# Performance work log

Measured on AMD Instinct MI355X. Metric: run time of the kernel, lower is better.

Reference implementation:

```python
import jax, jax.numpy as jnp
import numpy as np

ALPHA = 100.0
EPS = 1e-12  # matches torch F.normalize eps


def l2norm(v, axis):
    n = jnp.linalg.norm(v, axis=axis, keepdims=True)
    return v / jnp.maximum(n, EPS)


def setup_inputs() -> dict:
    key = jax.random.key(0)
    k1, k2 = jax.random.split(key)
    x = jax.random.normal(k1, (32, 512, 32, 32), dtype=jnp.float32)
    vocabs = jax.random.uniform(k2, (64, 512), dtype=jnp.float32)  # torch.rand init
    return {"x": x, "vocabs": vocabs}


def reference(x, vocabs):
    # x: [N, C, H, W]; vocabs: [K, C]
    N, C, H, W = x.shape
    K = vocabs.shape[0]
    x = l2norm(x, axis=1)                       # normalize descriptors over C
    xf = x.reshape(N, C, H * W)                 # [N, C, P]

    # 1x1 conv with weight = 2*alpha*vocabs, bias = -alpha*||vocabs||
    w = 2.0 * ALPHA * vocabs                    # [K, C]
    b = -ALPHA * jnp.linalg.norm(vocabs, axis=1)  # [K]
    logits = jnp.einsum('ncp,kc->nkp', xf, w) + b[None, :, None]
    a = jax.nn.softmax(logits, axis=1)          # soft assignment over K

    # Distributive rewrite of sum_p a[n,k,p]*(x[n,c,p] - vocabs[k,c])
    vlad = jnp.einsum('nkp,ncp->nkc', a, xf) - a.sum(-1)[:, :, None] * vocabs[None]
    vlad = l2norm(vlad, axis=2)                 # intra-normalization
    vlad = vlad.reshape(N, K * C)
    return l2norm(vlad, axis=1)
```

## Files before the change

### kernel.cpp

```cpp
#include <hip/hip_runtime.h>
#include <math.h>
#include <stdint.h>

#define ALPHA 100.0f
#define EPSN 1e-12f

typedef __attribute__((ext_vector_type(8))) short bf16x8;
typedef __attribute__((ext_vector_type(16))) float f32x16;
typedef __attribute__((ext_vector_type(4))) float f32x4;
typedef __attribute__((ext_vector_type(4))) unsigned int u32x4;

static __device__ __forceinline__ uint32_t f2bf(float f) {
    uint32_t u = __builtin_bit_cast(uint32_t, f);
    return (u + 0x7FFFu + ((u >> 16) & 1u)) >> 16;
}
static __device__ __forceinline__ float bfhi(uint32_t u) {
    return __builtin_bit_cast(float, u & 0xFFFF0000u);
}
static __device__ __forceinline__ uint32_t packbf(float a, float b) {
    return f2bf(a) | (f2bf(b) << 16);
}
static __device__ __forceinline__ void lds_barrier() {
    asm volatile("s_waitcnt lgkmcnt(0)\n\ts_barrier" ::: "memory");
}

__global__ __launch_bounds__(64) void prep_kernel(const float* __restrict__ v,
                                                  unsigned short* __restrict__ vh,
                                                  unsigned short* __restrict__ vl,
                                                  float* __restrict__ bias,
                                                  float* __restrict__ az) {
    int k = blockIdx.x, lane = threadIdx.x;
    az[k * 64 + lane] = 0.f;
    const float* row = v + k * 512;
    float ssq = 0.f;
#pragma unroll
    for (int i = 0; i < 8; ++i) {
        int c = lane + 64 * i;
        float f = row[c];
        ssq = fmaf(f, f, ssq);
        uint32_t hi = f2bf(f);
        uint32_t lo = f2bf(f - __builtin_bit_cast(float, hi << 16));
        vh[k * 512 + c] = (unsigned short)hi;
        vl[k * 512 + c] = (unsigned short)lo;
    }
#pragma unroll
    for (int off = 32; off > 0; off >>= 1) ssq += __shfl_xor(ssq, off, 64);
    if (lane == 0) bias[k] = -ALPHA * sqrtf(ssq);
}

__global__ __launch_bounds__(256) void assign_kernel(
    const float* __restrict__ x, const unsigned short* __restrict__ vh,
    const unsigned short* __restrict__ vl, const float* __restrict__ bias,
    unsigned short* __restrict__ aT, float* __restrict__ asum) {
    __shared__ uint32_t xph[4][2][16 * 36];
    __shared__ uint32_t xpl[4][2][16 * 36];
    __shared__ float ssqw[4][32];
    __shared__ float bias_l[64];
    __shared__ float xch[2][2][32];

    int tid = threadIdx.x, bx = blockIdx.x;
    int n = bx >> 4, pblk = (bx & 15) << 6;
    int l = tid & 63, w = tid >> 6;
    int kh = w & 1, ph = w >> 1;
    int h = l >> 5, cl = l & 31;
    int c8 = l & 7, j = (l >> 3) & 7;

    if (tid < 64) bias_l[tid] = bias[tid];

    const float* xg = x + (size_t)n * 524288 + pblk + 32 * ph + 4 * c8;
    const unsigned short* vhg = vh + (size_t)(32 * kh + cl) * 512 + 8 * h;
    const unsigned short* vlg = vl + (size_t)(32 * kh + cl) * 512 + 8 * h;

    uint32_t* bh0 = xph[w][0];
    uint32_t* bh1 = xph[w][1];
    uint32_t* bl0 = xpl[w][0];
    uint32_t* bl1 = xpl[w][1];

    f32x16 acc;
#pragma unroll
    for (int r = 0; r < 16; ++r) acc[r] = 0.f;
    f32x4 ssqv;
#pragma unroll
    for (int i = 0; i < 4; ++i) ssqv[i] = 0.f;

    float4 xv[2][4];
    u32x4 vfh[2][2], vfl[2][2];

#define A_LOADX(slot, c0)                                                      \
    {                                                                          \
        xv[slot][0] = *(const float4*)(xg + (size_t)((c0) + 2 * j) * 1024);    \
        xv[slot][1] = *(const float4*)(xg + (size_t)((c0) + 2 * j + 1) * 1024);\
        xv[slot][2] = *(const float4*)(xg + (size_t)((c0) + 2 * j + 16) * 1024);\
        xv[slot][3] = *(const float4*)(xg + (size_t)((c0) + 2 * j + 17) * 1024);\
    }
#define A_LOADV(slot, c0)                                                      \
    {                                                                          \
        vfh[slot][0] = *(const u32x4*)(vhg + (c0));                            \
        vfh[slot][1] = *(const u32x4*)(vhg + (c0) + 16);                       \
        vfl[slot][0] = *(const u32x4*)(vlg + (c0));                            \
        vfl[slot][1] = *(const u32x4*)(vlg + (c0) + 16);                       \
    }
#define A_STAGE(bh_, bl_, slot)                                                \
    {                                                                          \
        _Pragma("unroll") for (int ps0 = 0; ps0 < 2; ++ps0) {                  \
            float fa[4] = {xv[slot][2 * ps0].x, xv[slot][2 * ps0].y,           \
                           xv[slot][2 * ps0].z, xv[slot][2 * ps0].w};          \
            float fb[4] = {xv[slot][2 * ps0 + 1].x, xv[slot][2 * ps0 + 1].y,   \
                           xv[slot][2 * ps0 + 1].z, xv[slot][2 * ps0 + 1].w};  \
            u32x4 hp, lp;                                                      \
            _Pragma("unroll") for (int i = 0; i < 4; ++i) {                    \
                uint32_t h0 = f2bf(fa[i]);                                     \
                uint32_t l0 = f2bf(fa[i] - bfhi(h0 << 16));                    \
                uint32_t h1 = f2bf(fb[i]);                                     \
                uint32_t l1 = f2bf(fb[i] - bfhi(h1 << 16));                    \
                hp[i] = h0 | (h1 << 16);                                       \
                lp[i] = l0 | (l1 << 16);                                       \
                ssqv[i] = fmaf(fa[i], fa[i], fmaf(fb[i], fb[i], ssqv[i]));     \
            }                                                                  \
            *(u32x4*)&(bh_)[(j + 8 * ps0) * 36 + 4 * c8] = hp;                 \
            *(u32x4*)&(bl_)[(j + 8 * ps0) * 36 + 4 * c8] = lp;                 \
        }                                                                      \
    }
#define A_COMPUTE(bh_, bl_, slot)                                              \
    {                                                                          \
        _Pragma("unroll") for (int s = 0; s < 2; ++s) {                        \
            int xb = (8 * s + 4 * h) * 36 + cl;                                \
            u32x4 bhp, blp;                                                    \
            _Pragma("unroll") for (int q = 0; q < 4; ++q) {                    \
                bhp[q] = (bh_)[xb + q * 36];                                   \
                blp[q] = (bl_)[xb + q * 36];                                   \
            }                                                                  \
            bf16x8 ah = __builtin_bit_cast(bf16x8, vfh[slot][s]);              \
            bf16x8 al = __builtin_bit_cast(bf16x8, vfl[slot][s]);              \
            bf16x8 xbh = __builtin_bit_cast(bf16x8, bhp);                      \
            bf16x8 xbl = __builtin_bit_cast(bf16x8, blp);                      \
            acc = __builtin_amdgcn_mfma_f32_32x32x16_bf16(ah, xbh, acc, 0, 0, 0);\
            acc = __builtin_amdgcn_mfma_f32_32x32x16_bf16(ah, xbl, acc, 0, 0, 0);\
            acc = __builtin_amdgcn_mfma_f32_32x32x16_bf16(al, xbh, acc, 0, 0, 0);\
        }                                                                      \
    }

    A_LOADX(0, 0);
    A_LOADV(0, 0);
    A_LOADX(1, 32);
    A_LOADV(1, 32);
    __syncthreads();
    A_STAGE(bh0, bl0, 0);
#pragma unroll
    for (int i = 0; i < 16; ++i) {
        if ((i & 1) == 0) {
            A_COMPUTE(bh0, bl0, 0);
            if (i < 15) A_STAGE(bh1, bl1, 1);
            if (i < 14) {
                A_LOADX(0, (i + 2) * 32);
                A_LOADV(0, (i + 2) * 32);
            }
        } else {
            A_COMPUTE(bh1, bl1, 1);
            if (i < 15) A_STAGE(bh0, bl0, 0);
            if (i < 14) {
                A_LOADX(1, (i + 2) * 32);
                A_LOADV(1, (i + 2) * 32);
            }
        }
    }
#undef A_LOADX
#undef A_LOADV
#undef A_STAGE
#undef A_COMPUTE

#pragma unroll
    for (int i = 0; i < 4; ++i) {
        float v = ssqv[i];
        v += __shfl_xor(v, 8, 64);
        v += __shfl_xor(v, 16, 64);
        v += __shfl_xor(v, 32, 64);
        ssqv[i] = v;
    }
    if (l < 8) *(f32x4*)&ssqw[w][4 * c8] = ssqv;
    float ssq = ssqw[w][cl];

    float sinv = 1.0f / fmaxf(sqrtf(ssq), EPSN);
    float twoAs = 2.0f * ALPHA * sinv;
    float e[16];
    float m = -INFINITY;
#pragma unroll
    for (int r = 0; r < 16; ++r) {
        int k = (r & 3) + 8 * (r >> 2) + 4 * h + 32 * kh;
        float lv = fmaf(twoAs, acc[r], bias_l[k]);
        e[r] = lv;
        m = fmaxf(m, lv);
    }
    m = fmaxf(m, __shfl_xor(m, 32, 64));
    __syncthreads();
    if (l < 32) xch[kh][ph][l] = m;
    __syncthreads();
    m = fmaxf(m, xch[1 - kh][ph][cl]);
    float ssum = 0.f;
#pragma unroll
    for (int r = 0; r < 16; ++r) {
        e[r] = expf(e[r] - m);
        ssum += e[r];
    }
    ssum += __shfl_xor(ssum, 32, 64);
    __syncthreads();
    if (l < 32) xch[kh][ph][l] = ssum;
    __syncthreads();
    ssum += xch[1 - kh][ph][cl];
    float rs = 1.0f / ssum;
    float a2s = rs * sinv;
    unsigned short* aTn = aT + (size_t)n * 65536 + pblk + 32 * ph + cl;
#pragma unroll
    for (int r = 0; r < 16; ++r) {
        int k = (r & 3) + 8 * (r >> 2) + 4 * h + 32 * kh;
        aTn[(size_t)k * 1024] = (unsigned short)f2bf(e[r] * a2s);
        float red = e[r] * rs;
#pragma unroll
        for (int off = 1; off <= 16; off <<= 1) red += __shfl_xor(red, off, 64);
        if (cl == 0) atomicAdd(&asum[n * 64 + k], red);
    }
}

static __device__ __forceinline__ void v_load(float4& qxa, float4& qxb,
                                              u32x4& qa0, u32x4& qa1,
                                              const float* xg,
                                              const unsigned short* ag, int p0) {
    qxa = *(const float4*)(xg + p0);
    qxb = *(const float4*)(xg + p0 + 32);
    qa0 = *(const u32x4*)(ag + p0);
    qa1 = *(const u32x4*)(ag + p0 + 8);
}
static __device__ __forceinline__ void v_stage(uint32_t* xtb, uint32_t* atb,
                                               const float4 qxa, const float4 qxb,
                                               const u32x4 qa0, const u32x4 qa1,
                                               int xr, int xq, int ak, int aj) {
    int xb = xr * 34 + (xq >> 1);
    *(uint2*)&xtb[xb] = make_uint2(packbf(qxa.x, qxa.y), packbf(qxa.z, qxa.w));
    *(uint2*)&xtb[xb + 16] = make_uint2(packbf(qxb.x, qxb.y), packbf(qxb.z, qxb.w));
    int ab = ak * 34 + (aj >> 1);
    *(uint2*)&atb[ab] = make_uint2(qa0[0], qa0[1]);
    *(uint2*)&atb[ab + 2] = make_uint2(qa0[2], qa0[3]);
    *(uint2*)&atb[ab + 4] = make_uint2(qa1[0], qa1[1]);
    *(uint2*)&atb[ab + 6] = make_uint2(qa1[2], qa1[3]);
}
static __device__ __forceinline__ void v_compute(const uint32_t* xtb,
                                                 const uint32_t* atb,
                                                 f32x16& acc, int kh, int h,
                                                 int cl) {
#pragma unroll
    for (int s = 0; s < 4; ++s) {
        int va = (32 * kh + cl) * 34 + 8 * s + 4 * h;
        uint2 f0 = *(const uint2*)&atb[va];
        uint2 f1 = *(const uint2*)&atb[va + 2];
        int vb = cl * 34 + 8 * s + 4 * h;
        uint2 g0 = *(const uint2*)&xtb[vb];
        uint2 g1 = *(const uint2*)&xtb[vb + 2];
        u32x4 afp, bfp;
        afp[0] = f0.x; afp[1] = f0.y; afp[2] = f1.x; afp[3] = f1.y;
        bfp[0] = g0.x; bfp[1] = g0.y; bfp[2] = g1.x; bfp[3] = g1.y;
        acc = __builtin_amdgcn_mfma_f32_32x32x16_bf16(
            __builtin_bit_cast(bf16x8, afp), __builtin_bit_cast(bf16x8, bfp),
            acc, 0, 0, 0);
    }
}

__global__ __launch_bounds__(256) void vlad_kernel(
    const float* __restrict__ x, const unsigned short* __restrict__ aT,
    const float* __restrict__ asum, const float* __restrict__ vocabs,
    float* __restrict__ out, float* __restrict__ knorm) {
    __shared__ uint32_t xt[2][32 * 34];
    __shared__ uint32_t at[2][64 * 34];
    __shared__ float cmb[2][64][16];
    __shared__ float asum_l[64];

    int tid = threadIdx.x, bx = blockIdx.x;
    int n = bx >> 4, cb = (bx & 15) << 5;
    int l = tid & 63, w = tid >> 6;
    int kh = w & 1, ps = w >> 1;
    int h = l >> 5, cl = l & 31;

    if (tid < 64) asum_l[tid] = asum[n * 64 + tid];

    int xr = tid >> 3, xq = (tid & 7) << 2;
    int ak = tid >> 2, aj = (tid & 3) << 4;

    const float* xg = x + (size_t)n * 524288 + (size_t)(cb + xr) * 1024 + xq;
    const unsigned short* ag = aT + (size_t)n * 65536 + (size_t)ak * 1024 + aj;

    f32x16 acc;
#pragma unroll
    for (int r = 0; r < 16; ++r) acc[r] = 0.f;

    float4 qxa[2], qxb[2];
    u32x4 qa0[2], qa1[2];
    v_load(qxa[0], qxb[0], qa0[0], qa1[0], xg, ag, 0);
    v_load(qxa[1], qxb[1], qa0[1], qa1[1], xg, ag, 64);
    __syncthreads();
    v_stage(xt[0], at[0], qxa[0], qxb[0], qa0[0], qa1[0], xr, xq, ak, aj);
    lds_barrier();
#pragma unroll
    for (int cc = 0; cc < 8; ++cc) {
        v_stage(xt[1], at[1], qxa[1], qxb[1], qa0[1], qa1[1], xr, xq, ak, aj);
        if (cc < 7)
            v_load(qxa[0], qxb[0], qa0[0], qa1[0], xg, ag, (2 * cc + 2) << 6);
        if (ps == 0) v_compute(xt[0], at[0], acc, kh, h, cl);
        lds_barrier();
        if (cc < 7) {
            v_stage(xt[0], at[0], qxa[0], qxb[0], qa0[0], qa1[0], xr, xq, ak, aj);
            v_load(qxa[1], qxb[1], qa0[1], qa1[1], xg, ag, (2 * cc + 3) << 6);
        }
        if (ps == 1) v_compute(xt[1], at[1], acc, kh, h, cl);
        lds_barrier();
    }
    __syncthreads();
    if (ps == 1) {
#pragma unroll
        for (int r = 0; r < 16; ++r) cmb[kh][l][r] = acc[r];
    }
    __syncthreads();
    if (ps == 0) {
#pragma unroll
        for (int r = 0; r < 16; ++r) {
            int k = (r & 3) + 8 * (r >> 2) + 4 * h + 32 * kh;
            int c = cb + cl;
            float val = acc[r] + cmb[kh][l][r];
            val = fmaf(-asum_l[k], vocabs[k * 512 + c], val);
            out[(size_t)n * 32768 + (size_t)k * 512 + c] = val;
            float t2 = val * val;
#pragma unroll
            for (int off = 1; off <= 16; off <<= 1) t2 += __shfl_xor(t2, off, 64);
            if (cl == 0) atomicAdd(&knorm[n * 64 + k], t2);
        }
    }
}

__global__ __launch_bounds__(256) void scale_kernel(float* __restrict__ out,
                                                    const float* __restrict__ knorm) {
    int n = blockIdx.y;
    int sb = blockIdx.x;
    int tid = threadIdx.x;
    __shared__ float sc[64];
    __shared__ float tots;
    if (tid < 64) {
        float kn = knorm[n * 64 + tid];
        float nk = sqrtf(kn);
        float inv = 1.0f / fmaxf(nk, EPSN);
        sc[tid] = inv;
        float t = nk * inv;
        float t2 = t * t;
#pragma unroll
        for (int off = 32; off > 0; off >>= 1) t2 += __shfl_xor(t2, off, 64);
        if (tid == 0) tots = t2;
    }
    __syncthreads();
    float invt = 1.0f / fmaxf(sqrtf(tots), EPSN);
    float* base = out + (size_t)n * 32768 + sb * 4096;
#pragma unroll
    for (int i = 0; i < 16; ++i) {
        int idx = tid + 256 * i;
        int k = (sb * 4096 + idx) >> 9;
        base[idx] *= sc[k] * invt;
    }
}

extern "C" void kernel_launch(void* const* d_in, const int* in_sizes, int n_in,
                              void* d_out, int out_size, void* d_ws, size_t ws_size,
                              hipStream_t stream) {
    const float* x = (const float*)d_in[0];
    const float* vocabs = (const float*)d_in[1];
    float* out = (float*)d_out;
    char* ws = (char*)d_ws;
    unsigned short* vh = (unsigned short*)(ws);
    unsigned short* vl = (unsigned short*)(ws + 65536);
    float* bias  = (float*)(ws + 131072);
    float* asum  = (float*)(ws + 131328);
    float* knorm = (float*)(ws + 139520);
    unsigned short* aT = (unsigned short*)(ws + 147712);

    prep_kernel<<<64, 64, 0, stream>>>(vocabs, vh, vl, bias, asum);
    assign_kernel<<<512, 256, 0, stream>>>(x, vh, vl, bias, aT, asum);
    vlad_kernel<<<512, 256, 0, stream>>>(x, aT, asum, vocabs, out, knorm);
    scale_kernel<<<dim3(8, 32), 256, 0, stream>>>(out, knorm);
}
```

Before: 149.5 us.

## Split channel reduction across waves in assign and vlad kernels, double blocks/threads

```diff
diff --git a/kernel.cpp b/kernel.cpp
--- a/kernel.cpp
+++ b/kernel.cpp
@@ -52,117 +52,125 @@
     const float* __restrict__ x, const unsigned short* __restrict__ vh,
     const unsigned short* __restrict__ vl, const float* __restrict__ bias,
     unsigned short* __restrict__ aT, float* __restrict__ asum) {
-    __shared__ uint32_t xph[4][2][16 * 36];
-    __shared__ uint32_t xpl[4][2][16 * 36];
-    __shared__ float ssqw[4][32];
+    __shared__ uint32_t xsh[2][2][16 * 36];
+    __shared__ uint32_t xsl[2][2][16 * 36];
+    __shared__ float cmb[2][64][17];
+    __shared__ float __attribute__((aligned(16))) ssq_w[4][32];
     __shared__ float bias_l[64];
-    __shared__ float xch[2][2][32];
+    __shared__ float xchm[2][32];
+    __shared__ float xchs[2][32];
 
     int tid = threadIdx.x, bx = blockIdx.x;
-    int n = bx >> 4, pblk = (bx & 15) << 6;
+    int n = bx >> 5, pblk = (bx & 31) << 5;
     int l = tid & 63, w = tid >> 6;
-    int kh = w & 1, ph = w >> 1;
+    int kh = w & 1, ch = w >> 1;
     int h = l >> 5, cl = l & 31;
-    int c8 = l & 7, j = (l >> 3) & 7;
+    int sid = kh * 64 + l;
+    int j = sid >> 3, q = sid & 7;
 
     if (tid < 64) bias_l[tid] = bias[tid];
 
-    const float* xg = x + (size_t)n * 524288 + pblk + 32 * ph + 4 * c8;
-    const unsigned short* vhg = vh + (size_t)(32 * kh + cl) * 512 + 8 * h;
-    const unsigned short* vlg = vl + (size_t)(32 * kh + cl) * 512 + 8 * h;
-
-    uint32_t* bh0 = xph[w][0];
-    uint32_t* bh1 = xph[w][1];
-    uint32_t* bl0 = xpl[w][0];
-    uint32_t* bl1 = xpl[w][1];
-
-    f32x16 acc;
-#pragma unroll
-    for (int r = 0; r < 16; ++r) acc[r] = 0.f;
+    const float* xg = x + (size_t)n * 524288 + (size_t)(ch * 256 + 2 * j) * 1024 +
+                      pblk + 4 * q;
+    const unsigned short* vhg = vh + (size_t)(32 * kh + cl) * 512 + ch * 256 + 8 * h;
+    const unsigned short* vlg = vl + (size_t)(32 * kh + cl) * 512 + ch * 256 + 8 * h;
+
+    f32x16 accA, accB;
+#pragma unroll
+    for (int r = 0; r < 16; ++r) { accA[r] = 0.f; accB[r] = 0.f; }
     f32x4 ssqv;
 #pragma unroll
     for (int i = 0; i < 4; ++i) ssqv[i] = 0.f;
 
-    float4 xv[2][4];
+    float4 xv[2][2];
     u32x4 vfh[2][2], vfl[2][2];
 
-#define A_LOADX(slot, c0)                                                      \
-    {                                                                          \
-        xv[slot][0] = *(const float4*)(xg + (size_t)((c0) + 2 * j) * 1024);    \
-        xv[slot][1] = *(const float4*)(xg + (size_t)((c0) + 2 * j + 1) * 1024);\
-        xv[slot][2] = *(const float4*)(xg + (size_t)((c0) + 2 * j + 16) * 1024);\
-        xv[slot][3] = *(const float4*)(xg + (size_t)((c0) + 2 * j + 17) * 1024);\
-    }
-#define A_LOADV(slot, c0)                                                      \
-    {                                                                          \
-        vfh[slot][0] = *(const u32x4*)(vhg + (c0));                            \
-        vfh[slot][1] = *(const u32x4*)(vhg + (c0) + 16);                       \
-        vfl[slot][0] = *(const u32x4*)(vlg + (c0));                            \
-        vfl[slot][1] = *(const u32x4*)(vlg + (c0) + 16);                       \
-    }
-#define A_STAGE(bh_, bl_, slot)                                                \
-    {                                                                          \
-        _Pragma("unroll") for (int ps0 = 0; ps0 < 2; ++ps0) {                  \
-            float fa[4] = {xv[slot][2 * ps0].x, xv[slot][2 * ps0].y,           \
-                           xv[slot][2 * ps0].z, xv[slot][2 * ps0].w};          \
-            float fb[4] = {xv[slot][2 * ps0 + 1].x, xv[slot][2 * ps0 + 1].y,   \
-                           xv[slot][2 * ps0 + 1].z, xv[slot][2 * ps0 + 1].w};  \
-            u32x4 hp, lp;                                                      \
-            _Pragma("unroll") for (int i = 0; i < 4; ++i) {                    \
-                uint32_t h0 = f2bf(fa[i]);                                     \
-                uint32_t l0 = f2bf(fa[i] - bfhi(h0 << 16));                    \
-                uint32_t h1 = f2bf(fb[i]);                                     \
-                uint32_t l1 = f2bf(fb[i] - bfhi(h1 << 16));                    \
-                hp[i] = h0 | (h1 << 16);                                       \
-                lp[i] = l0 | (l1 << 16);                                       \
-                ssqv[i] = fmaf(fa[i], fa[i], fmaf(fb[i], fb[i], ssqv[i]));     \
+#define A_LOADX(slot, cc)                                                      \
+    do {                                                                       \
+        const float* p_ = xg + (size_t)(cc)*32768;                             \
+        xv[slot][0] = *(const float4*)p_;                                      \
+        xv[slot][1] = *(const float4*)(p_ + 1024);                             \
+    } while (0)
+#define A_LOADV(slot, cc)                                                      \
+    do {                                                                       \
+        vfh[slot][0] = *(const u32x4*)(vhg + (cc)*32);                         \
+        vfh[slot][1] = *(const u32x4*)(vhg + (cc)*32 + 16);                    \
+        vfl[slot][0] = *(const u32x4*)(vlg + (cc)*32);                         \
+        vfl[slot][1] = *(const u32x4*)(vlg + (cc)*32 + 16);                    \
+    } while (0)
+#define A_STAGE(buf, slot)                                                     \
+    do {                                                                       \
+        float fa[4] = {xv[slot][0].x, xv[slot][0].y, xv[slot][0].z,            \
+                       xv[slot][0].w};                                         \
+        float fb[4] = {xv[slot][1].x, xv[slot][1].y, xv[slot][1].z,            \
+                       xv[slot][1].w};                                         \
+        u32x4 hp, lp;                                                          \
+        _Pragma("unroll") for (int i = 0; i < 4; ++i) {                        \
+            uint32_t h0 = f2bf(fa[i]);                                         \
+            uint32_t l0 = f2bf(fa[i] - bfhi(h0 << 16));                        \
+            uint32_t h1 = f2bf(fb[i]);                                         \
+            uint32_t l1 = f2bf(fb[i] - bfhi(h1 << 16));                        \
+            hp[i] = h0 | (h1 << 16);                                           \
+            lp[i] = l0 | (l1 << 16);                                           \
+            ssqv[i] = fmaf(fa[i], fa[i], fmaf(fb[i], fb[i], ssqv[i]));         \
+        }                                                                      \
+        *(u32x4*)&xsh[ch][buf][j * 36 + 4 * q] = hp;                           \
+        *(u32x4*)&xsl[ch][buf][j * 36 + 4 * q] = lp;                           \
+    } while (0)
+#define A_COMPUTE(buf, slot)                                                   \
+    do {                                                                       \
+        {                                                   \
+            int xb = (4 * h) * 36 + cl;                                        \
+            u32x4 bhp, blp;                                                    \
+            _Pragma("unroll") for (int q2 = 0; q2 < 4; ++q2) {                 \
+                bhp[q2] = xsh[ch][buf][xb + q2 * 36];                          \
+                blp[q2] = xsl[ch][buf][xb + q2 * 36];                          \
             }                                                                  \
-            *(u32x4*)&(bh_)[(j + 8 * ps0) * 36 + 4 * c8] = hp;                 \
-            *(u32x4*)&(bl_)[(j + 8 * ps0) * 36 + 4 * c8] = lp;                 \
+            bf16x8 ah = __builtin_bit_cast(bf16x8, vfh[slot][0]);              \
+            bf16x8 al = __builtin_bit_cast(bf16x8, vfl[slot][0]);              \
+            bf16x8 xh = __builtin_bit_cast(bf16x8, bhp);                       \
+            bf16x8 xl = __builtin_bit_cast(bf16x8, blp);                       \
+            accA = __builtin_amdgcn_mfma_f32_32x32x16_bf16(ah, xh, accA, 0, 0, 0);\
+            accA = __builtin_amdgcn_mfma_f32_32x32x16_bf16(ah, xl, accA, 0, 0, 0);\
+            accA = __builtin_amdgcn_mfma_f32_32x32x16_bf16(al, xh, accA, 0, 0, 0);\
         }                                                                      \
-    }
-#define A_COMPUTE(bh_, bl_, slot)                                              \
-    {                                                                          \
-        _Pragma("unroll") for (int s = 0; s < 2; ++s) {                        \
-            int xb = (8 * s + 4 * h) * 36 + cl;                                \
+        {                                                   \
+            int xb = (8 + 4 * h) * 36 + cl;                                    \
             u32x4 bhp, blp;                                                    \
-            _Pragma("unroll") for (int q = 0; q < 4; ++q) {                    \
-                bhp[q] = (bh_)[xb + q * 36];                                   \
-                blp[q] = (bl_)[xb + q * 36];                                   \
+            _Pragma("unroll") for (int q2 = 0; q2 < 4; ++q2) {                 \
+                bhp[q2] = xsh[ch][buf][xb + q2 * 36];                          \
+                blp[q2] = xsl[ch][buf][xb + q2 * 36];                          \
             }                                                                  \
-            bf16x8 ah = __builtin_bit_cast(bf16x8, vfh[slot][s]);              \
-            bf16x8 al = __builtin_bit_cast(bf16x8, vfl[slot][s]);              \
-            bf16x8 xbh = __builtin_bit_cast(bf16x8, bhp);                      \
-            bf16x8 xbl = __builtin_bit_cast(bf16x8, blp);                      \
-            acc = __builtin_amdgcn_mfma_f32_32x32x16_bf16(ah, xbh, acc, 0, 0, 0);\
-            acc = __builtin_amdgcn_mfma_f32_32x32x16_bf16(ah, xbl, acc, 0, 0, 0);\
-            acc = __builtin_amdgcn_mfma_f32_32x32x16_bf16(al, xbh, acc, 0, 0, 0);\
+            bf16x8 ah = __builtin_bit_cast(bf16x8, vfh[slot][1]);              \
+            bf16x8 al = __builtin_bit_cast(bf16x8, vfl[slot][1]);              \
+            bf16x8 xh = __builtin_bit_cast(bf16x8, bhp);                       \
+            bf16x8 xl = __builtin_bit_cast(bf16x8, blp);                       \
+            accB = __builtin_amdgcn_mfma_f32_32x32x16_bf16(ah, xh, accB, 0, 0, 0);\
+            accB = __builtin_amdgcn_mfma_f32_32x32x16_bf16(ah, xl, accB, 0, 0, 0);\
+            accB = __builtin_amdgcn_mfma_f32_32x32x16_bf16(al, xh, accB, 0, 0, 0);\
         }                                                                      \
-    }
+    } while (0)
 
     A_LOADX(0, 0);
     A_LOADV(0, 0);
-    A_LOADX(1, 32);
-    A_LOADV(1, 32);
-    __syncthreads();
-    A_STAGE(bh0, bl0, 0);
-#pragma unroll
-    for (int i = 0; i < 16; ++i) {
-        if ((i & 1) == 0) {
-            A_COMPUTE(bh0, bl0, 0);
-            if (i < 15) A_STAGE(bh1, bl1, 1);
-            if (i < 14) {
-                A_LOADX(0, (i + 2) * 32);
-                A_LOADV(0, (i + 2) * 32);
-            }
-        } else {
-            A_COMPUTE(bh1, bl1, 1);
-            if (i < 15) A_STAGE(bh0, bl0, 0);
-            if (i < 14) {
-                A_LOADX(1, (i + 2) * 32);
-                A_LOADV(1, (i + 2) * 32);
-            }
-        }
+    A_LOADX(1, 1);
+    A_LOADV(1, 1);
+    A_STAGE(0, 0);
+    lds_barrier();
+#pragma unroll
+    for (int cc = 0; cc < 8; ++cc) {
+        int cur = cc & 1;
+        if (cc < 7) {
+            if (cur == 0) A_STAGE(1, 1);
+            else A_STAGE(0, 0);
+        }
+        if (cur == 0) A_COMPUTE(0, 0);
+        else A_COMPUTE(1, 1);
+        if (cc < 6) {
+            if (cur == 0) { A_LOADX(0, cc + 2); A_LOADV(0, cc + 2); }
+            else          { A_LOADX(1, cc + 2); A_LOADV(1, cc + 2); }
+        }
+        lds_barrier();
     }
 #undef A_LOADX
 #undef A_LOADV
@@ -177,100 +185,65 @@
         v += __shfl_xor(v, 32, 64);
         ssqv[i] = v;
     }
-    if (l < 8) *(f32x4*)&ssqw[w][4 * c8] = ssqv;
-    float ssq = ssqw[w][cl];
-
-    float sinv = 1.0f / fmaxf(sqrtf(ssq), EPSN);
-    float twoAs = 2.0f * ALPHA * sinv;
-    float e[16];
-    float m = -INFINITY;
-#pragma unroll
-    for (int r = 0; r < 16; ++r) {
-        int k = (r & 3) + 8 * (r >> 2) + 4 * h + 32 * kh;
-        float lv = fmaf(twoAs, acc[r], bias_l[k]);
-        e[r] = lv;
-        m = fmaxf(m, lv);
-    }
-    m = fmaxf(m, __shfl_xor(m, 32, 64));
-    __syncthreads();
-    if (l < 32) xch[kh][ph][l] = m;
-    __syncthreads();
-    m = fmaxf(m, xch[1 - kh][ph][cl]);
-    float ssum = 0.f;
-#pragma unroll
-    for (int r = 0; r < 16; ++r) {
-        e[r] = expf(e[r] - m);
-        ssum += e[r];
-    }
-    ssum += __shfl_xor(ssum, 32, 64);
-    __syncthreads();
-    if (l < 32) xch[kh][ph][l] = ssum;
-    __syncthreads();
-    ssum += xch[1 - kh][ph][cl];
-    float rs = 1.0f / ssum;
-    float a2s = rs * sinv;
-    unsigned short* aTn = aT + (size_t)n * 65536 + pblk + 32 * ph + cl;
-#pragma unroll
-    for (int r = 0; r < 16; ++r) {
-        int k = (r & 3) + 8 * (r >> 2) + 4 * h + 32 * kh;
-        aTn[(size_t)k * 1024] = (unsigned short)f2bf(e[r] * a2s);
-        float red = e[r] * rs;
-#pragma unroll
-        for (int off = 1; off <= 16; off <<= 1) red += __shfl_xor(red, off, 64);
-        if (cl == 0) atomicAdd(&asum[n * 64 + k], red);
-    }
-}
-
-static __device__ __forceinline__ void v_load(float4& qxa, float4& qxb,
-                                              u32x4& qa0, u32x4& qa1,
-                                              const float* xg,
-                                              const unsigned short* ag, int p0) {
-    qxa = *(const float4*)(xg + p0);
-    qxb = *(const float4*)(xg + p0 + 32);
-    qa0 = *(const u32x4*)(ag + p0);
-    qa1 = *(const u32x4*)(ag + p0 + 8);
-}
-static __device__ __forceinline__ void v_stage(uint32_t* xtb, uint32_t* atb,
-                                               const float4 qxa, const float4 qxb,
-                                               const u32x4 qa0, const u32x4 qa1,
-                                               int xr, int xq, int ak, int aj) {
-    int xb = xr * 34 + (xq >> 1);
-    *(uint2*)&xtb[xb] = make_uint2(packbf(qxa.x, qxa.y), packbf(qxa.z, qxa.w));
-    *(uint2*)&xtb[xb + 16] = make_uint2(packbf(qxb.x, qxb.y), packbf(qxb.z, qxb.w));
-    int ab = ak * 34 + (aj >> 1);
-    *(uint2*)&atb[ab] = make_uint2(qa0[0], qa0[1]);
-    *(uint2*)&atb[ab + 2] = make_uint2(qa0[2], qa0[3]);
-    *(uint2*)&atb[ab + 4] = make_uint2(qa1[0], qa1[1]);
-    *(uint2*)&atb[ab + 6] = make_uint2(qa1[2], qa1[3]);
-}
-static __device__ __forceinline__ void v_compute(const uint32_t* xtb,
-                                                 const uint32_t* atb,
-                                                 f32x16& acc, int kh, int h,
-                                                 int cl) {
-#pragma unroll
-    for (int s = 0; s < 4; ++s) {
-        int va = (32 * kh + cl) * 34 + 8 * s + 4 * h;
-        uint2 f0 = *(const uint2*)&atb[va];
-        uint2 f1 = *(const uint2*)&atb[va + 2];
-        int vb = cl * 34 + 8 * s + 4 * h;
-        uint2 g0 = *(const uint2*)&xtb[vb];
-        uint2 g1 = *(const uint2*)&xtb[vb + 2];
-        u32x4 afp, bfp;
-        afp[0] = f0.x; afp[1] = f0.y; afp[2] = f1.x; afp[3] = f1.y;
-        bfp[0] = g0.x; bfp[1] = g0.y; bfp[2] = g1.x; bfp[3] = g1.y;
-        acc = __builtin_amdgcn_mfma_f32_32x32x16_bf16(
-            __builtin_bit_cast(bf16x8, afp), __builtin_bit_cast(bf16x8, bfp),
-            acc, 0, 0, 0);
-    }
-}
-
-__global__ __launch_bounds__(256) void vlad_kernel(
+    if (l < 8) *(f32x4*)&ssq_w[w][4 * l] = ssqv;
+    if (ch == 1) {
+#pragma unroll
+        for (int r = 0; r < 16; ++r) cmb[kh][l][r] = accA[r] + accB[r];
+    }
+    __syncthreads();
+
+    float m = -INFINITY, ssum = 0.f, sinv = 0.f, e[16];
+    if (ch == 0) {
+        float ssq = ssq_w[0][cl] + ssq_w[1][cl] + ssq_w[2][cl] + ssq_w[3][cl];
+        sinv = 1.0f / fmaxf(sqrtf(ssq), EPSN);
+        float twoAs = 2.0f * ALPHA * sinv;
+#pragma unroll
+        for (int r = 0; r < 16; ++r) {
+            int k = (r & 3) + 8 * (r >> 2) + 4 * h + 32 * kh;
+            float dv = accA[r] + accB[r] + cmb[kh][l][r];
+            float lv = fmaf(twoAs, dv, bias_l[k]);
+            e[r] = lv;
+            m = fmaxf(m, lv);
+        }
+        m = fmaxf(m, __shfl_xor(m, 32, 64));
+    }
+    if (ch == 0 && l < 32) xchm[kh][l] = m;
+    __syncthreads();
+    if (ch == 0) {
+        m = fmaxf(m, xchm[1 - kh][cl]);
+#pragma unroll
+        for (int r = 0; r < 16; ++r) {
+            e[r] = expf(e[r] - m);
+            ssum += e[r];
+        }
+        ssum += __shfl_xor(ssum, 32, 64);
+    }
+    if (ch == 0 && l < 32) xchs[kh][l] = ssum;
+    __syncthreads();
+    if (ch == 0) {
+        ssum += xchs[1 - kh][cl];
+        float rs = 1.0f / ssum;
+        float a2s = rs * sinv;
+        unsigned short* aTn = aT + (size_t)n * 65536 + pblk + cl;
+#pragma unroll
+        for (int r = 0; r < 16; ++r) {
+            int k = (r & 3) + 8 * (r >> 2) + 4 * h + 32 * kh;
+            aTn[(size_t)k * 1024] = (unsigned short)f2bf(e[r] * a2s);
+            float red = e[r] * rs;
+#pragma unroll
+            for (int off = 1; off <= 16; off <<= 1) red += __shfl_xor(red, off, 64);
+            if (cl == 0) atomicAdd(&asum[n * 64 + k], red);
+        }
+    }
+}
+
+__global__ __launch_bounds__(512) void vlad_kernel(
     const float* __restrict__ x, const unsigned short* __restrict__ aT,
     const float* __restrict__ asum, const float* __restrict__ vocabs,
     float* __restrict__ out, float* __restrict__ knorm) {
     __shared__ uint32_t xt[2][32 * 34];
     __shared__ uint32_t at[2][64 * 34];
-    __shared__ float cmb[2][64][16];
+    __shared__ float cmb[3][2][64][17];
     __shared__ float asum_l[64];
 
     int tid = threadIdx.x, bx = blockIdx.x;
@@ -281,41 +254,81 @@
 
     if (tid < 64) asum_l[tid] = asum[n * 64 + tid];
 
-    int xr = tid >> 3, xq = (tid & 7) << 2;
-    int ak = tid >> 2, aj = (tid & 3) << 4;
-
-    const float* xg = x + (size_t)n * 524288 + (size_t)(cb + xr) * 1024 + xq;
-    const unsigned short* ag = aT + (size_t)n * 65536 + (size_t)ak * 1024 + aj;
-
-    f32x16 acc;
-#pragma unroll
-    for (int r = 0; r < 16; ++r) acc[r] = 0.f;
-
-    float4 qxa[2], qxb[2];
-    u32x4 qa0[2], qa1[2];
-    v_load(qxa[0], qxb[0], qa0[0], qa1[0], xg, ag, 0);
-    v_load(qxa[1], qxb[1], qa0[1], qa1[1], xg, ag, 64);
-    __syncthreads();
-    v_stage(xt[0], at[0], qxa[0], qxb[0], qa0[0], qa1[0], xr, xq, ak, aj);
+    int xr = tid >> 4, xq = tid & 15;
+    int ak = tid >> 3, aq = tid & 7;
+
+    const float* xg = x + (size_t)n * 524288 + (size_t)(cb + xr) * 1024 + 4 * xq;
+    const unsigned short* ag = aT + (size_t)n * 65536 + (size_t)ak * 1024 + 8 * aq;
+
+    f32x16 accA, accB;
+#pragma unroll
+    for (int r = 0; r < 16; ++r) { accA[r] = 0.f; accB[r] = 0.f; }
+
+    float4 qx[2];
+    u32x4 qa[2];
+
+#define V_LOAD(slot, chk)                                                      \
+    do {                                                                       \
+        qx[slot] = *(const float4*)(xg + (chk)*64);                            \
+        qa[slot] = *(const u32x4*)(ag + (chk)*64);                             \
+    } while (0)
+#define V_STAGE(buf, slot)                                                     \
+    do {                                                                       \
+        *(uint2*)&xt[buf][xr * 34 + 2 * xq] =                                  \
+            make_uint2(packbf(qx[slot].x, qx[slot].y),                         \
+                       packbf(qx[slot].z, qx[slot].w));                        \
+        *(uint2*)&at[buf][ak * 34 + 4 * aq] =                                  \
+            make_uint2(qa[slot][0], qa[slot][1]);                              \
+        *(uint2*)&at[buf][ak * 34 + 4 * aq + 2] =                              \
+            make_uint2(qa[slot][2], qa[slot][3]);                              \
+    } while (0)
+#define V_COMP(buf)                                                            \
+    do {                                                                       \
+        _Pragma("unroll") for (int s = 0; s < 4; ++s) {                        \
+            int va = (32 * kh + cl) * 34 + 8 * s + 4 * h;                      \
+            uint2 f0 = *(const uint2*)&at[buf][va];                            \
+            uint2 f1 = *(const uint2*)&at[buf][va + 2];                        \
+            int vb = cl * 34 + 8 * s + 4 * h;                                  \
+            uint2 g0 = *(const uint2*)&xt[buf][vb];                            \
+            uint2 g1 = *(const uint2*)&xt[buf][vb + 2];                        \
+            u32x4 afp, bfp;                                                    \
+            afp[0] = f0.x; afp[1] = f0.y; afp[2] = f1.x; afp[3] = f1.y;        \
+            bfp[0] = g0.x; bfp[1] = g0.y; bfp[2] = g1.x; bfp[3] = g1.y;        \
+            f32x16& accr = (s & 1) ? accB : accA;                              \
+            accr = __builtin_amdgcn_mfma_f32_32x32x16_bf16(                    \
+                __builtin_bit_cast(bf16x8, afp), __builtin_bit_cast(bf16x8, bfp),\
+                accr, 0, 0, 0);                                                \
+        }                                                                      \
+    } while (0)
+
+    V_LOAD(0, 0);
+    V_LOAD(1, 1);
+    V_STAGE(0, 0);
     lds_barrier();
 #pragma unroll
-    for (int cc = 0; cc < 8; ++cc) {
-        v_stage(xt[1], at[1], qxa[1], qxb[1], qa0[1], qa1[1], xr, xq, ak, aj);
-        if (cc < 7)
-            v_load(qxa[0], qxb[0], qa0[0], qa1[0], xg, ag, (2 * cc + 2) << 6);
-        if (ps == 0) v_compute(xt[0], at[0], acc, kh, h, cl);
+    for (int chk = 0; chk < 16; ++chk) {
+        int cur = chk & 1;
+        if (chk < 15) {
+            if (cur == 0) V_STAGE(1, 1);
+            else V_STAGE(0, 0);
+        }
+        if (ps == (chk & 3)) {
+            if (cur == 0) V_COMP(0);
+            else V_COMP(1);
+        }
+        if (chk < 14) {
+            if (cur == 0) V_LOAD(0, chk + 2);
+            else V_LOAD(1, chk + 2);
+        }
         lds_barrier();
-        if (cc < 7) {
-            v_stage(xt[0], at[0], qxa[0], qxb[0], qa0[0], qa1[0], xr, xq, ak, aj);
-            v_load(qxa[1], qxb[1], qa0[1], qa1[1], xg, ag, (2 * cc + 3) << 6);
-        }
-        if (ps == 1) v_compute(xt[1], at[1], acc, kh, h, cl);
-        lds_barrier();
-    }
-    __syncthreads();
-    if (ps == 1) {
-#pragma unroll
-        for (int r = 0; r < 16; ++r) cmb[kh][l][r] = acc[r];
+    }
+#undef V_LOAD
+#undef V_STAGE
+#undef V_COMP
+
+    if (ps != 0) {
+#pragma unroll
+        for (int r = 0; r < 16; ++r) cmb[ps - 1][kh][l][r] = accA[r] + accB[r];
     }
     __syncthreads();
     if (ps == 0) {
@@ -323,7 +336,8 @@
         for (int r = 0; r < 16; ++r) {
             int k = (r & 3) + 8 * (r >> 2) + 4 * h + 32 * kh;
             int c = cb + cl;
-            float val = acc[r] + cmb[kh][l][r];
+            float val = accA[r] + accB[r] + cmb[0][kh][l][r] + cmb[1][kh][l][r] +
+                        cmb[2][kh][l][r];
             val = fmaf(-asum_l[k], vocabs[k * 512 + c], val);
             out[(size_t)n * 32768 + (size_t)k * 512 + c] = val;
             float t2 = val * val;
@@ -378,7 +392,7 @@
     unsigned short* aT = (unsigned short*)(ws + 147712);
 
     prep_kernel<<<64, 64, 0, stream>>>(vocabs, vh, vl, bias, asum);
-    assign_kernel<<<512, 256, 0, stream>>>(x, vh, vl, bias, aT, asum);
-    vlad_kernel<<<512, 256, 0, stream>>>(x, aT, asum, vocabs, out, knorm);
+    assign_kernel<<<1024, 256, 0, stream>>>(x, vh, vl, bias, aT, asum);
+    vlad_kernel<<<512, 512, 0, stream>>>(x, aT, asum, vocabs, out, knorm);
     scale_kernel<<<dim3(8, 32), 256, 0, stream>>>(out, knorm);
 }
```

Result: no change. 149.7 us (+0.1%).

## Restructure assign kernel with shared block-wide x staging and triple-buffered loads

Applied to the files above, without the earlier changes.

```diff
diff --git a/kernel.cpp b/kernel.cpp
--- a/kernel.cpp
+++ b/kernel.cpp
@@ -48,173 +48,146 @@
     if (lane == 0) bias[k] = -ALPHA * sqrtf(ssq);
 }
 
-__global__ __launch_bounds__(256) void assign_kernel(
+__global__ __launch_bounds__(512) void assign_kernel(
     const float* __restrict__ x, const unsigned short* __restrict__ vh,
     const unsigned short* __restrict__ vl, const float* __restrict__ bias,
     unsigned short* __restrict__ aT, float* __restrict__ asum) {
-    __shared__ uint32_t xph[4][2][16 * 36];
-    __shared__ uint32_t xpl[4][2][16 * 36];
-    __shared__ float ssqw[4][32];
+    __shared__ uint32_t xsh[2][16 * 132];
+    __shared__ uint32_t xsl[2][16 * 132];
+    __shared__ float ssq_s[16][132];
+    __shared__ float ssq_l[128];
     __shared__ float bias_l[64];
-    __shared__ float xch[2][2][32];
+    __shared__ float xchm[4][2][32];
+    __shared__ float xchs[4][2][32];
 
     int tid = threadIdx.x, bx = blockIdx.x;
-    int n = bx >> 4, pblk = (bx & 15) << 6;
+    int n = bx >> 3, pblk = (bx & 7) << 7;
     int l = tid & 63, w = tid >> 6;
-    int kh = w & 1, ph = w >> 1;
+    int kh = w & 1, ps = w >> 1;
     int h = l >> 5, cl = l & 31;
-    int c8 = l & 7, j = (l >> 3) & 7;
+    int r = tid >> 5, q = tid & 31;
 
     if (tid < 64) bias_l[tid] = bias[tid];
 
-    const float* xg = x + (size_t)n * 524288 + pblk + 32 * ph + 4 * c8;
+    const float* xg = x + (size_t)n * 524288 + (size_t)(2 * r) * 1024 + pblk + 4 * q;
     const unsigned short* vhg = vh + (size_t)(32 * kh + cl) * 512 + 8 * h;
     const unsigned short* vlg = vl + (size_t)(32 * kh + cl) * 512 + 8 * h;
 
-    uint32_t* bh0 = xph[w][0];
-    uint32_t* bh1 = xph[w][1];
-    uint32_t* bl0 = xpl[w][0];
-    uint32_t* bl1 = xpl[w][1];
-
-    f32x16 acc;
-#pragma unroll
-    for (int r = 0; r < 16; ++r) acc[r] = 0.f;
+    f32x16 accA, accB;
+#pragma unroll
+    for (int i = 0; i < 16; ++i) { accA[i] = 0.f; accB[i] = 0.f; }
     f32x4 ssqv;
 #pragma unroll
     for (int i = 0; i < 4; ++i) ssqv[i] = 0.f;
 
-    float4 xv[2][4];
-    u32x4 vfh[2][2], vfl[2][2];
-
-#define A_LOADX(slot, c0)                                                      \
-    {                                                                          \
-        xv[slot][0] = *(const float4*)(xg + (size_t)((c0) + 2 * j) * 1024);    \
-        xv[slot][1] = *(const float4*)(xg + (size_t)((c0) + 2 * j + 1) * 1024);\
-        xv[slot][2] = *(const float4*)(xg + (size_t)((c0) + 2 * j + 16) * 1024);\
-        xv[slot][3] = *(const float4*)(xg + (size_t)((c0) + 2 * j + 17) * 1024);\
-    }
-#define A_LOADV(slot, c0)                                                      \
-    {                                                                          \
-        vfh[slot][0] = *(const u32x4*)(vhg + (c0));                            \
-        vfh[slot][1] = *(const u32x4*)(vhg + (c0) + 16);                       \
-        vfl[slot][0] = *(const u32x4*)(vlg + (c0));                            \
-        vfl[slot][1] = *(const u32x4*)(vlg + (c0) + 16);                       \
-    }
-#define A_STAGE(bh_, bl_, slot)                                                \
-    {                                                                          \
-        _Pragma("unroll") for (int ps0 = 0; ps0 < 2; ++ps0) {                  \
-            float fa[4] = {xv[slot][2 * ps0].x, xv[slot][2 * ps0].y,           \
-                           xv[slot][2 * ps0].z, xv[slot][2 * ps0].w};          \
-            float fb[4] = {xv[slot][2 * ps0 + 1].x, xv[slot][2 * ps0 + 1].y,   \
-                           xv[slot][2 * ps0 + 1].z, xv[slot][2 * ps0 + 1].w};  \
-            u32x4 hp, lp;                                                      \
-            _Pragma("unroll") for (int i = 0; i < 4; ++i) {                    \
-                uint32_t h0 = f2bf(fa[i]);                                     \
-                uint32_t l0 = f2bf(fa[i] - bfhi(h0 << 16));                    \
-                uint32_t h1 = f2bf(fb[i]);                                     \
-                uint32_t l1 = f2bf(fb[i] - bfhi(h1 << 16));                    \
-                hp[i] = h0 | (h1 << 16);                                       \
-                lp[i] = l0 | (l1 << 16);                                       \
-                ssqv[i] = fmaf(fa[i], fa[i], fmaf(fb[i], fb[i], ssqv[i]));     \
-            }                                                                  \
-            *(u32x4*)&(bh_)[(j + 8 * ps0) * 36 + 4 * c8] = hp;                 \
-            *(u32x4*)&(bl_)[(j + 8 * ps0) * 36 + 4 * c8] = lp;                 \
+    float4 xa[3], xb[3];
+    u32x4 vfh[3][2], vfl[3][2];
+
+#define A_LOAD(slot, cc)                                                       \
+    do {                                                                       \
+        xa[slot] = *(const float4*)(xg + (size_t)(cc)*32768);                  \
+        xb[slot] = *(const float4*)(xg + (size_t)(cc)*32768 + 1024);           \
+        vfh[slot][0] = *(const u32x4*)(vhg + (cc)*32);                         \
+        vfh[slot][1] = *(const u32x4*)(vhg + (cc)*32 + 16);                    \
+        vfl[slot][0] = *(const u32x4*)(vlg + (cc)*32);                         \
+        vfl[slot][1] = *(const u32x4*)(vlg + (cc)*32 + 16);                    \
+    } while (0)
+#define A_STAGE(buf, slot)                                                     \
+    do {                                                                       \
+        float fa[4] = {xa[slot].x, xa[slot].y, xa[slot].z, xa[slot].w};        \
+        float fb[4] = {xb[slot].x, xb[slot].y, xb[slot].z, xb[slot].w};        \
+        u32x4 hp, lp;                                                          \
+        _Pragma("unroll") for (int i = 0; i < 4; ++i) {                        \
+            uint32_t h0 = f2bf(fa[i]);                                         \
+            uint32_t l0 = f2bf(fa[i] - bfhi(h0 << 16));                        \
+            uint32_t h1 = f2bf(fb[i]);                                         \
+            uint32_t l1 = f2bf(fb[i] - bfhi(h1 << 16));                        \
+            hp[i] = h0 | (h1 << 16);                                           \
+            lp[i] = l0 | (l1 << 16);                                           \
+            ssqv[i] = fmaf(fa[i], fa[i], fmaf(fb[i], fb[i], ssqv[i]));         \
         }                                                                      \
-    }
-#define A_COMPUTE(bh_, bl_, slot)                                              \
-    {                                                                          \
+        *(u32x4*)&xsh[buf][r * 132 + 4 * q] = hp;                              \
+        *(u32x4*)&xsl[buf][r * 132 + 4 * q] = lp;                              \
+    } while (0)
+#define A_COMPUTE(buf, slot)                                                   \
+    do {                                                                       \
         _Pragma("unroll") for (int s = 0; s < 2; ++s) {                        \
-            int xb = (8 * s + 4 * h) * 36 + cl;                                \
+            int xb_ = (8 * s + 4 * h) * 132 + 32 * ps + cl;                    \
             u32x4 bhp, blp;                                                    \
-            _Pragma("unroll") for (int q = 0; q < 4; ++q) {                    \
-                bhp[q] = (bh_)[xb + q * 36];                                   \
-                blp[q] = (bl_)[xb + q * 36];                                   \
+            _Pragma("unroll") for (int q2 = 0; q2 < 4; ++q2) {                 \
+                bhp[q2] = xsh[buf][xb_ + q2 * 132];                            \
+                blp[q2] = xsl[buf][xb_ + q2 * 132];                            \
             }                                                                  \
             bf16x8 ah = __builtin_bit_cast(bf16x8, vfh[slot][s]);              \
             bf16x8 al = __builtin_bit_cast(bf16x8, vfl[slot][s]);              \
-            bf16x8 xbh = __builtin_bit_cast(bf16x8, bhp);                      \
-            bf16x8 xbl = __builtin_bit_cast(bf16x8, blp);                      \
-            acc = __builtin_amdgcn_mfma_f32_32x32x16_bf16(ah, xbh, acc, 0, 0, 0);\
-            acc = __builtin_amdgcn_mfma_f32_32x32x16_bf16(ah, xbl, acc, 0, 0, 0);\
-            acc = __builtin_amdgcn_mfma_f32_32x32x16_bf16(al, xbh, acc, 0, 0, 0);\
+            bf16x8 xh_ = __builtin_bit_cast(bf16x8, bhp);                      \
+            bf16x8 xl_ = __builtin_bit_cast(bf16x8, blp);                      \
+            f32x16& accr = s ? accB : accA;                                    \
+            accr = __builtin_amdgcn_mfma_f32_32x32x16_bf16(ah, xh_, accr, 0, 0, 0);\
+            accr = __builtin_amdgcn_mfma_f32_32x32x16_bf16(ah, xl_, accr, 0, 0, 0);\
+            accr = __builtin_amdgcn_mfma_f32_32x32x16_bf16(al, xh_, accr, 0, 0, 0);\
         }                                                                      \
-    }
-
-    A_LOADX(0, 0);
-    A_LOADV(0, 0);
-    A_LOADX(1, 32);
-    A_LOADV(1, 32);
-    __syncthreads();
-    A_STAGE(bh0, bl0, 0);
-#pragma unroll
-    for (int i = 0; i < 16; ++i) {
-        if ((i & 1) == 0) {
-            A_COMPUTE(bh0, bl0, 0);
-            if (i < 15) A_STAGE(bh1, bl1, 1);
-            if (i < 14) {
-                A_LOADX(0, (i + 2) * 32);
-                A_LOADV(0, (i + 2) * 32);
-            }
-        } else {
-            A_COMPUTE(bh1, bl1, 1);
-            if (i < 15) A_STAGE(bh0, bl0, 0);
-            if (i < 14) {
-                A_LOADX(1, (i + 2) * 32);
-                A_LOADV(1, (i + 2) * 32);
-            }
-        }
-    }
-#undef A_LOADX
-#undef A_LOADV
+    } while (0)
+
+    A_LOAD(0, 0);
+    A_LOAD(1, 1);
+    A_LOAD(2, 2);
+    A_STAGE(0, 0);
+    lds_barrier();
+#pragma unroll
+    for (int cc = 0; cc < 16; ++cc) {
+        if (cc < 15) A_STAGE((cc + 1) & 1, (cc + 1) % 3);
+        A_COMPUTE(cc & 1, cc % 3);
+        if (cc < 13) A_LOAD(cc % 3, cc + 3);
+        lds_barrier();
+    }
+#undef A_LOAD
 #undef A_STAGE
 #undef A_COMPUTE
 
-#pragma unroll
-    for (int i = 0; i < 4; ++i) {
-        float v = ssqv[i];
-        v += __shfl_xor(v, 8, 64);
-        v += __shfl_xor(v, 16, 64);
-        v += __shfl_xor(v, 32, 64);
-        ssqv[i] = v;
-    }
-    if (l < 8) *(f32x4*)&ssqw[w][4 * c8] = ssqv;
-    float ssq = ssqw[w][cl];
-
+    *(f32x4*)&ssq_s[r][4 * q] = ssqv;
+    __syncthreads();
+    if (tid < 128) {
+        float s = 0.f;
+#pragma unroll
+        for (int rr = 0; rr < 16; ++rr) s += ssq_s[rr][tid];
+        ssq_l[tid] = s;
+    }
+    __syncthreads();
+    float ssq = ssq_l[32 * ps + cl];
     float sinv = 1.0f / fmaxf(sqrtf(ssq), EPSN);
     float twoAs = 2.0f * ALPHA * sinv;
     float e[16];
     float m = -INFINITY;
 #pragma unroll
-    for (int r = 0; r < 16; ++r) {
-        int k = (r & 3) + 8 * (r >> 2) + 4 * h + 32 * kh;
-        float lv = fmaf(twoAs, acc[r], bias_l[k]);
-        e[r] = lv;
+    for (int rr = 0; rr < 16; ++rr) {
+        int k = (rr & 3) + 8 * (rr >> 2) + 4 * h + 32 * kh;
+        float lv = fmaf(twoAs, accA[rr] + accB[rr], bias_l[k]);
+        e[rr] = lv;
         m = fmaxf(m, lv);
     }
     m = fmaxf(m, __shfl_xor(m, 32, 64));
-    __syncthreads();
-    if (l < 32) xch[kh][ph][l] = m;
-    __syncthreads();
-    m = fmaxf(m, xch[1 - kh][ph][cl]);
+    if (l < 32) xchm[ps][kh][l] = m;
+    __syncthreads();
+    m = fmaxf(m, xchm[ps][1 - kh][cl]);
     float ssum = 0.f;
 #pragma unroll
-    for (int r = 0; r < 16; ++r) {
-        e[r] = expf(e[r] - m);
-        ssum += e[r];
+    for (int rr = 0; rr < 16; ++rr) {
+        e[rr] = expf(e[rr] - m);
+        ssum += e[rr];
     }
     ssum += __shfl_xor(ssum, 32, 64);
-    __syncthreads();
-    if (l < 32) xch[kh][ph][l] = ssum;
-    __syncthreads();
-    ssum += xch[1 - kh][ph][cl];
+    if (l < 32) xchs[ps][kh][l] = ssum;
+    __syncthreads();
+    ssum += xchs[ps][1 - kh][cl];
     float rs = 1.0f / ssum;
     float a2s = rs * sinv;
-    unsigned short* aTn = aT + (size_t)n * 65536 + pblk + 32 * ph + cl;
-#pragma unroll
-    for (int r = 0; r < 16; ++r) {
-        int k = (r & 3) + 8 * (r >> 2) + 4 * h + 32 * kh;
-        aTn[(size_t)k * 1024] = (unsigned short)f2bf(e[r] * a2s);
-        float red = e[r] * rs;
+    unsigned short* aTn = aT + (size_t)n * 65536 + pblk + 32 * ps + cl;
+#pragma unroll
+    for (int rr = 0; rr < 16; ++rr) {
+        int k = (rr & 3) + 8 * (rr >> 2) + 4 * h + 32 * kh;
+        aTn[(size_t)k * 1024] = (unsigned short)f2bf(e[rr] * a2s);
+        float red = e[rr] * rs;
 #pragma unroll
         for (int off = 1; off <= 16; off <<= 1) red += __shfl_xor(red, off, 64);
         if (cl == 0) atomicAdd(&asum[n * 64 + k], red);
@@ -289,7 +262,7 @@
 
     f32x16 acc;
 #pragma unroll
-    for (int r = 0; r < 16; ++r) acc[r] = 0.f;
+    for (int i = 0; i < 16; ++i) acc[i] = 0.f;
 
     float4 qxa[2], qxb[2];
     u32x4 qa0[2], qa1[2];
@@ -315,15 +288,15 @@
     __syncthreads();
     if (ps == 1) {
 #pragma unroll
-        for (int r = 0; r < 16; ++r) cmb[kh][l][r] = acc[r];
+        for (int i = 0; i < 16; ++i) cmb[kh][l][i] = acc[i];
     }
     __syncthreads();
     if (ps == 0) {
 #pragma unroll
-        for (int r = 0; r < 16; ++r) {
-            int k = (r & 3) + 8 * (r >> 2) + 4 * h + 32 * kh;
+        for (int i = 0; i < 16; ++i) {
+            int k = (i & 3) + 8 * (i >> 2) + 4 * h + 32 * kh;
             int c = cb + cl;
-            float val = acc[r] + cmb[kh][l][r];
+            float val = acc[i] + cmb[kh][l][i];
             val = fmaf(-asum_l[k], vocabs[k * 512 + c], val);
             out[(size_t)n * 32768 + (size_t)k * 512 + c] = val;
             float t2 = val * val;
@@ -378,7 +351,7 @@
     unsigned short* aT = (unsigned short*)(ws + 147712);
 
     prep_kernel<<<64, 64, 0, stream>>>(vocabs, vh, vl, bias, asum);
-    assign_kernel<<<512, 256, 0, stream>>>(x, vh, vl, bias, aT, asum);
+    assign_kernel<<<256, 512, 0, stream>>>(x, vh, vl, bias, aT, asum);
     vlad_kernel<<<512, 256, 0, stream>>>(x, aT, asum, vocabs, out, knorm);
     scale_kernel<<<dim3(8, 32), 256, 0, stream>>>(out, knorm);
 }
```

Result: faster. 144.2 us (-3.5%).
